# Kernel tuning notes

Hardware: AMD Instinct MI355X
Metric: run time of the kernel (lower is better)

Reference implementation:

```python
import jax, jax.numpy as jnp
import numpy as np
import math

IN_FEATURES = 3072
PADDED = 4096  # next power of two
ACT_BITS = 8
LN_EPS = 1e-6


def hadamard_transform(x):
    """Normalized fast Walsh-Hadamard transform along last dim (power of 2)."""
    n = x.shape[-1]
    m = n.bit_length() - 1  # log2(n)
    shape = x.shape
    y = x.reshape(shape[:-1] + (2,) * m)
    for ax in range(len(shape) - 1, len(shape) - 1 + m):
        a = jnp.take(y, 0, axis=ax)
        b = jnp.take(y, 1, axis=ax)
        y = jnp.stack([a + b, a - b], axis=ax)
    return y.reshape(shape) / jnp.sqrt(jnp.asarray(n, x.dtype))


def activation_quant(x, bits=ACT_BITS):
    """Per-token absmax int-b quant with STE (BitNet style)."""
    qb = 2 ** (bits - 1) - 1  # 127
    scale = qb / jnp.clip(jnp.max(jnp.abs(x), axis=-1, keepdims=True), 1e-5)
    q = jnp.clip(jnp.round(x * scale), -qb - 1, qb) / scale
    return x + jax.lax.stop_gradient(q - x)


def weight_quant(w):
    """Ternary absmean weight quant with STE (as in training path)."""
    scale = jnp.clip(jnp.mean(jnp.abs(w)), 1e-5)
    q = jnp.clip(jnp.round(w / scale), -1.0, 1.0) * scale
    return w + jax.lax.stop_gradient(q - w)


def layer_norm(x, gamma, beta, eps=LN_EPS):
    mu = jnp.mean(x, axis=-1, keepdims=True)
    var = jnp.mean(jnp.square(x - mu), axis=-1, keepdims=True)
    return (x - mu) * jax.lax.rsqrt(var + eps) * gamma + beta


def setup_inputs() -> dict:
    key = jax.random.key(0)
    k1, k2 = jax.random.split(key)
    x = jax.random.normal(k1, (4, 2048, IN_FEATURES), dtype=jnp.float32)
    ln_gamma = jnp.ones((IN_FEATURES,), dtype=jnp.float32)
    ln_beta = jnp.zeros((IN_FEATURES,), dtype=jnp.float32)
    weight = jax.random.normal(k2, (4096, PADDED), dtype=jnp.float32) * 0.02
    return {"x": x, "ln_gamma": ln_gamma, "ln_beta": ln_beta, "weight": weight}


def reference(x, ln_gamma, ln_beta, weight):
    x_norm = layer_norm(x, ln_gamma, ln_beta)
    pad = PADDED - IN_FEATURES
    x_pad = jnp.pad(x_norm, ((0, 0), (0, 0), (0, pad)))
    x_had = hadamard_transform(x_pad)
    x_q = activation_quant(x_had)
    w_q = weight_quant(weight)
    # F.linear: x @ W^T
    out = jnp.einsum('bsd,od->bso', x_q, w_q)
    return out
```

## Files before the change

### kernel.cpp

```cpp
#include <hip/hip_runtime.h>
#include <stdint.h>

#define TOKENS 8192
#define IN_F   3072
#define PAD_F  4096
#define N_OUT  4096
#define K_DIM  4096

using i32x4 = __attribute__((ext_vector_type(4))) int;

#define Q_OFF    0
#define WQ_OFF   33554432
#define AINV_OFF 50331648
#define PART_OFF 50364416
#define WSC_OFF  50380800

__device__ __forceinline__ void gload_lds16(const void* g, void* l) {
    __builtin_amdgcn_global_load_lds(
        (__attribute__((address_space(1))) void*)(void*)g,
        (__attribute__((address_space(3))) void*)l,
        16, 0, 0);
}

__global__ __launch_bounds__(256) void k_wabs(const float* __restrict__ w,
                                              float* __restrict__ partial) {
    int tid = threadIdx.x;
    const float4* w4 = (const float4*)(w + (size_t)blockIdx.x * 4096);
    float s = 0.f;
#pragma unroll
    for (int i = 0; i < 4; ++i) {
        float4 v = w4[tid + i * 256];
        s += fabsf(v.x) + fabsf(v.y) + fabsf(v.z) + fabsf(v.w);
    }
#pragma unroll
    for (int o = 32; o > 0; o >>= 1) s += __shfl_xor(s, o);
    __shared__ float rb[4];
    if ((tid & 63) == 0) rb[tid >> 6] = s;
    __syncthreads();
    if (tid == 0) partial[blockIdx.x] = rb[0] + rb[1] + rb[2] + rb[3];
}

__global__ __launch_bounds__(256) void k_wscale(const float* __restrict__ partial,
                                                float* __restrict__ wsp) {
    int tid = threadIdx.x;
    float s = 0.f;
#pragma unroll
    for (int i = 0; i < 16; ++i) s += partial[tid + i * 256];
#pragma unroll
    for (int o = 32; o > 0; o >>= 1) s += __shfl_xor(s, o);
    __shared__ float rb[4];
    if ((tid & 63) == 0) rb[tid >> 6] = s;
    __syncthreads();
    if (tid == 0)
        wsp[0] = fmaxf((rb[0] + rb[1] + rb[2] + rb[3]) * (1.0f / 16777216.0f), 1e-5f);
}

__global__ __launch_bounds__(256) void k_wquant(const float* __restrict__ w,
                                                const float* __restrict__ wsp,
                                                unsigned int* __restrict__ wq) {
    int idx = blockIdx.x * 256 + threadIdx.x;
    float ws = wsp[0];
    float4 v = ((const float4*)w)[idx];
    int a = (int)rintf(v.x / ws); a = max(-1, min(1, a));
    int b = (int)rintf(v.y / ws); b = max(-1, min(1, b));
    int c = (int)rintf(v.z / ws); c = max(-1, min(1, c));
    int d = (int)rintf(v.w / ws); d = max(-1, min(1, d));
    unsigned int p = (unsigned)(a & 255) | ((unsigned)(b & 255) << 8) |
                     ((unsigned)(c & 255) << 16) | ((unsigned)(d & 255) << 24);
    wq[idx] = p;
}

__global__ __launch_bounds__(256) void k_lnfwht(const float* __restrict__ x,
                                                const float* __restrict__ gamma,
                                                const float* __restrict__ beta,
                                                signed char* __restrict__ q,
                                                float* __restrict__ ainv) {
    __shared__ float s[PAD_F];
    __shared__ float rb[8];
    int tid = threadIdx.x;
    int lane = tid & 63;
    int t = blockIdx.x;
    const float4* xr4 = (const float4*)(x + (size_t)t * IN_F);
    const float4* g4  = (const float4*)gamma;
    const float4* b4  = (const float4*)beta;

    float v[16];
    float sum = 0.f;
#pragma unroll
    for (int i = 0; i < 3; ++i) {
        float4 xv = xr4[tid + i * 256];
        v[4 * i + 0] = xv.x; v[4 * i + 1] = xv.y;
        v[4 * i + 2] = xv.z; v[4 * i + 3] = xv.w;
        sum += xv.x + xv.y + xv.z + xv.w;
    }
    v[12] = v[13] = v[14] = v[15] = 0.f;
#pragma unroll
    for (int o = 32; o > 0; o >>= 1) sum += __shfl_xor(sum, o);
    if (lane == 0) rb[tid >> 6] = sum;
    __syncthreads();
    float mu = (rb[0] + rb[1] + rb[2] + rb[3]) * (1.0f / 3072.0f);

    float s2 = 0.f;
#pragma unroll
    for (int i = 0; i < 12; ++i) { float d = v[i] - mu; s2 += d * d; }
#pragma unroll
    for (int o = 32; o > 0; o >>= 1) s2 += __shfl_xor(s2, o);
    if (lane == 0) rb[4 + (tid >> 6)] = s2;
    __syncthreads();
    float var = (rb[4] + rb[5] + rb[6] + rb[7]) * (1.0f / 3072.0f);
    float rstd = 1.0f / sqrtf(var + 1e-6f);

#pragma unroll
    for (int i = 0; i < 3; ++i) {
        float4 gv = g4[tid + i * 256];
        float4 bv = b4[tid + i * 256];
        v[4 * i + 0] = (v[4 * i + 0] - mu) * rstd * gv.x + bv.x;
        v[4 * i + 1] = (v[4 * i + 1] - mu) * rstd * gv.y + bv.y;
        v[4 * i + 2] = (v[4 * i + 2] - mu) * rstd * gv.z + bv.z;
        v[4 * i + 3] = (v[4 * i + 3] - mu) * rstd * gv.w + bv.w;
    }

#pragma unroll
    for (int i = 0; i < 4; ++i) {
        float a0 = v[4 * i], a1 = v[4 * i + 1], a2 = v[4 * i + 2], a3 = v[4 * i + 3];
        float t0 = a0 + a1, t1 = a0 - a1, t2 = a2 + a3, t3 = a2 - a3;
        v[4 * i] = t0 + t2; v[4 * i + 1] = t1 + t3;
        v[4 * i + 2] = t0 - t2; v[4 * i + 3] = t1 - t3;
    }
#pragma unroll
    for (int c = 0; c < 4; ++c) {
        float a0 = v[c], a1 = v[4 + c], a2 = v[8 + c], a3 = v[12 + c];
        float t0 = a0 + a1, t1 = a0 - a1, t2 = a2 + a3, t3 = a2 - a3;
        v[c] = t0 + t2; v[4 + c] = t1 + t3;
        v[8 + c] = t0 - t2; v[12 + c] = t1 - t3;
    }
#pragma unroll
    for (int m = 1; m <= 32; m <<= 1) {
#pragma unroll
        for (int r = 0; r < 16; ++r) {
            float p = __shfl_xor(v[r], m);
            v[r] = (lane & m) ? (p - v[r]) : (v[r] + p);
        }
    }
#pragma unroll
    for (int m = 64; m <= 128; m <<= 1) {
        __syncthreads();
#pragma unroll
        for (int r = 0; r < 16; ++r) s[r * 256 + tid] = v[r];
        __syncthreads();
#pragma unroll
        for (int r = 0; r < 16; ++r) {
            float p = s[r * 256 + (tid ^ m)];
            v[r] = (tid & m) ? (p - v[r]) : (v[r] + p);
        }
    }

    float mx = 0.f;
#pragma unroll
    for (int r = 0; r < 16; ++r) mx = fmaxf(mx, fabsf(v[r]));
#pragma unroll
    for (int o = 32; o > 0; o >>= 1) mx = fmaxf(mx, __shfl_xor(mx, o));
    __syncthreads();
    if (lane == 0) rb[tid >> 6] = mx;
    __syncthreads();
    float amraw = fmaxf(fmaxf(rb[0], rb[1]), fmaxf(rb[2], rb[3]));
    float amax = fmaxf(amraw * (1.0f / 64.0f), 1e-5f);
    float scale = 127.0f / amax;
    if (tid == 0) ainv[t] = amax * (1.0f / 127.0f);

    unsigned int* qr = (unsigned int*)(q + (size_t)t * PAD_F);
#pragma unroll
    for (int i = 0; i < 4; ++i) {
        unsigned int pk = 0;
#pragma unroll
        for (int c = 0; c < 4; ++c) {
            int qi = (int)rintf(v[4 * i + c] * (1.0f / 64.0f) * scale);
            qi = max(-128, min(127, qi));
            pk |= (unsigned)(qi & 255) << (8 * c);
        }
        qr[tid + i * 256] = pk;
    }
}

#define BK 64
#define NT (K_DIM / BK)

#define VMW(n) asm volatile("s_waitcnt vmcnt(" #n ")" ::: "memory")

__global__ __launch_bounds__(512, 2) void k_gemm(const signed char* __restrict__ Aq,
                                                 const signed char* __restrict__ Wq,
                                                 const float* __restrict__ ainv,
                                                 const float* __restrict__ wsp,
                                                 float* __restrict__ out) {
    __shared__ signed char sA[4][128 * 128];
    __shared__ signed char sB[4][128 * 128];

    int tid = threadIdx.x;
    int lane = tid & 63, wid = tid >> 6;

    int bid = blockIdx.x;
    int xcd = bid & 7, li = bid >> 3;
    int bmb = xcd * 4 + (li & 3);
    int bnb = li >> 2;
    size_t bm0 = (size_t)bmb * 256, bn0 = (size_t)bnb * 256;

    int wm = wid >> 2, wn = wid & 3;

    int rr = lane >> 3, pp = lane & 7;
    int Lg = pp ^ rr;
    int spar = Lg >> 2, sh = Lg & 3;
    const signed char* gA = Aq + (bm0 + (size_t)(wid * 32 + 2 * rr + spar)) * K_DIM + sh * 16;
    const signed char* gB = Wq + (bn0 + (size_t)(wid * 32 + 2 * rr + spar)) * K_DIM + sh * 16;

    int fr = lane & 15, hh = lane >> 4;
    int pos = (((fr & 1) << 2) | hh) ^ (fr >> 1);
    int abase = (wm * 64 + (fr >> 1)) * 8 + pos;
    int bbase = (wn * 32 + (fr >> 1)) * 8 + pos;

    i32x4 acc[8][4];
#pragma unroll
    for (int m = 0; m < 8; ++m)
#pragma unroll
        for (int n = 0; n < 4; ++n) acc[m][n] = (i32x4){0, 0, 0, 0};

    i32x4 afA[8], bfA[4], afB[8], bfB[4];

    auto STAGE = [&](int b, int t) {
        size_t k0 = (size_t)t * BK;
        gload_lds16(gA + k0, &sA[b][(wid * 16) * 128]);
        gload_lds16(gA + k0 + (size_t)16 * K_DIM, &sA[b][(wid * 16 + 8) * 128]);
        gload_lds16(gB + k0, &sB[b][(wid * 16) * 128]);
        gload_lds16(gB + k0 + (size_t)16 * K_DIM, &sB[b][(wid * 16 + 8) * 128]);
    };

#define LOADF(B, AF, BF) do {                                           \
    const i32x4* va = (const i32x4*)&sA[B][0];                          \
    const i32x4* vb = (const i32x4*)&sB[B][0];                          \
    _Pragma("unroll")                                                   \
    for (int mf = 0; mf < 8; ++mf) AF[mf] = va[abase + mf * 64];        \
    _Pragma("unroll")                                                   \
    for (int nf = 0; nf < 4; ++nf) BF[nf] = vb[bbase + nf * 64];        \
} while (0)

#define COMPUTE(AF, BF) do {                                            \
    __builtin_amdgcn_s_setprio(1);                                      \
    _Pragma("unroll")                                                   \
    for (int mf = 0; mf < 8; ++mf)                                      \
        _Pragma("unroll")                                               \
        for (int nf = 0; nf < 4; ++nf)                                  \
            acc[mf][nf] = __builtin_amdgcn_mfma_i32_16x16x64_i8(        \
                AF[mf], BF[nf], acc[mf][nf], 0, 0, 0);                  \
    __builtin_amdgcn_s_setprio(0);                                      \
} while (0)

#define BODY(T, AFC, BFC, AFN, BFN) do {                                \
    STAGE((T + 3) & 3, T + 3);                                          \
    VMW(8);                                                             \
    __builtin_amdgcn_sched_barrier(0);                                  \
    __builtin_amdgcn_s_barrier();                                       \
    __builtin_amdgcn_sched_barrier(0);                                  \
    LOADF((T + 1) & 3, AFN, BFN);                                       \
    COMPUTE(AFC, BFC);                                                  \
    asm volatile("s_waitcnt lgkmcnt(0)" ::: "memory");                  \
    __builtin_amdgcn_sched_barrier(0);                                  \
} while (0)

    STAGE(0, 0);
    STAGE(1, 1);
    STAGE(2, 2);
    VMW(8);
    __builtin_amdgcn_sched_barrier(0);
    __builtin_amdgcn_s_barrier();
    __builtin_amdgcn_sched_barrier(0);
    LOADF(0, afA, bfA);
    asm volatile("s_waitcnt lgkmcnt(0)" ::: "memory");
    __builtin_amdgcn_sched_barrier(0);

#pragma unroll 1
    for (int t = 0; t < NT - 4; t += 2) {
        BODY(t, afA, bfA, afB, bfB);
        BODY(t + 1, afB, bfB, afA, bfA);
    }
    BODY(NT - 4, afA, bfA, afB, bfB);
    VMW(4);
    __builtin_amdgcn_sched_barrier(0);
    __builtin_amdgcn_s_barrier();
    __builtin_amdgcn_sched_barrier(0);
    LOADF(2, afA, bfA);
    COMPUTE(afB, bfB);
    asm volatile("s_waitcnt lgkmcnt(0)" ::: "memory");
    __builtin_amdgcn_sched_barrier(0);
    VMW(0);
    __builtin_amdgcn_sched_barrier(0);
    __builtin_amdgcn_s_barrier();
    __builtin_amdgcn_sched_barrier(0);
    LOADF(3, afB, bfB);
    COMPUTE(afA, bfA);
    asm volatile("s_waitcnt lgkmcnt(0)" ::: "memory");
    __builtin_amdgcn_sched_barrier(0);
    COMPUTE(afB, bfB);

    float wsc = wsp[0];
#pragma unroll
    for (int mf = 0; mf < 8; ++mf) {
        size_t row0 = bm0 + wm * 128 + mf * 16 + hh * 4;
#pragma unroll
        for (int r = 0; r < 4; ++r) {
            size_t row = row0 + r;
            float sa = wsc * ainv[row];
#pragma unroll
            for (int nf = 0; nf < 4; ++nf) {
                size_t col = bn0 + wn * 64 + nf * 16 + fr;
                out[row * N_OUT + col] = (float)acc[mf][nf][r] * sa;
            }
        }
    }
#undef LOADF
#undef COMPUTE
#undef BODY
}

extern "C" void kernel_launch(void* const* d_in, const int* in_sizes, int n_in,
                              void* d_out, int out_size, void* d_ws, size_t ws_size,
                              hipStream_t stream) {
    const float* x     = (const float*)d_in[0];
    const float* gamma = (const float*)d_in[1];
    const float* beta  = (const float*)d_in[2];
    const float* w     = (const float*)d_in[3];
    float* out = (float*)d_out;
    char* ws = (char*)d_ws;

    signed char* q   = (signed char*)(ws + Q_OFF);
    signed char* wq  = (signed char*)(ws + WQ_OFF);
    float* ainv      = (float*)(ws + AINV_OFF);
    float* partial   = (float*)(ws + PART_OFF);
    float* wsp       = (float*)(ws + WSC_OFF);

    k_wabs<<<dim3(4096), dim3(256), 0, stream>>>(w, partial);
    k_wscale<<<dim3(1), dim3(256), 0, stream>>>(partial, wsp);
    k_wquant<<<dim3(16384), dim3(256), 0, stream>>>(w, wsp, (unsigned int*)wq);
    k_lnfwht<<<dim3(TOKENS), dim3(256), 0, stream>>>(x, gamma, beta, q, ainv);
    k_gemm<<<dim3(512), dim3(512), 0, stream>>>(q, wq, ainv, wsp, out);
}
```

Baseline: 212.6 us.

## Restructure int8 GEMM main loop into two half-phases with single fragment set

Replaces the double-buffered register-fragment pipeline (prefetching the next tile's LDS fragments during compute) with a per-tile schedule split into two phases. Each phase loads part of the B fragments and issues half of the global-to-LDS stage, then runs half of the MFMAs, with extra workgroup barriers in between. This halves fragment register usage, which may ease register pressure, and interleaves memory issue with compute at a finer grain. The cost is that LDS reads are no longer overlapped with the previous tile's MFMAs, and there are more barriers per iteration.

```diff
diff --git a/kernel.cpp b/kernel.cpp
--- a/kernel.cpp
+++ b/kernel.cpp
@@ -186,6 +186,7 @@
 #define NT (K_DIM / BK)
 
 #define VMW(n) asm volatile("s_waitcnt vmcnt(" #n ")" ::: "memory")
+#define SB0()  __builtin_amdgcn_sched_barrier(0)
 
 __global__ __launch_bounds__(512, 2) void k_gemm(const signed char* __restrict__ Aq,
                                                  const signed char* __restrict__ Wq,
@@ -223,7 +224,7 @@
 #pragma unroll
         for (int n = 0; n < 4; ++n) acc[m][n] = (i32x4){0, 0, 0, 0};
 
-    i32x4 afA[8], bfA[4], afB[8], bfB[4];
+    i32x4 af[8], bf[4];
 
     auto STAGE = [&](int b, int t) {
         size_t k0 = (size_t)t * BK;
@@ -233,72 +234,72 @@
         gload_lds16(gB + k0 + (size_t)16 * K_DIM, &sB[b][(wid * 16 + 8) * 128]);
     };
 
-#define LOADF(B, AF, BF) do {                                           \
-    const i32x4* va = (const i32x4*)&sA[B][0];                          \
-    const i32x4* vb = (const i32x4*)&sB[B][0];                          \
+#define BODY(T, N, DS) do {                                             \
+    const i32x4* va = (const i32x4*)&sA[(T) & 3][0];                    \
+    const i32x4* vb = (const i32x4*)&sB[(T) & 3][0];                    \
+                     \
     _Pragma("unroll")                                                   \
-    for (int mf = 0; mf < 8; ++mf) AF[mf] = va[abase + mf * 64];        \
-    _Pragma("unroll")                                                   \
-    for (int nf = 0; nf < 4; ++nf) BF[nf] = vb[bbase + nf * 64];        \
-} while (0)
-
-#define COMPUTE(AF, BF) do {                                            \
+    for (int mf = 0; mf < 8; ++mf) af[mf] = va[abase + mf * 64];        \
+    bf[0] = vb[bbase];                                                  \
+    bf[1] = vb[bbase + 64];                                             \
+    if (DS) {                                                           \
+        size_t k0 = (size_t)((T) + 3) * BK;                             \
+        gload_lds16(gA + k0, &sA[((T) + 3) & 3][(wid * 16) * 128]);     \
+        gload_lds16(gA + k0 + (size_t)16 * K_DIM,                       \
+                    &sA[((T) + 3) & 3][(wid * 16 + 8) * 128]);          \
+    }                                                                   \
+    SB0();                                                              \
+    __builtin_amdgcn_s_barrier();                                       \
+    asm volatile("s_waitcnt lgkmcnt(0)" ::: "memory");                  \
+    SB0();                                                              \
     __builtin_amdgcn_s_setprio(1);                                      \
     _Pragma("unroll")                                                   \
-    for (int mf = 0; mf < 8; ++mf)                                      \
-        _Pragma("unroll")                                               \
-        for (int nf = 0; nf < 4; ++nf)                                  \
-            acc[mf][nf] = __builtin_amdgcn_mfma_i32_16x16x64_i8(        \
-                AF[mf], BF[nf], acc[mf][nf], 0, 0, 0);                  \
+    for (int mf = 0; mf < 8; ++mf) {                                    \
+        acc[mf][0] = __builtin_amdgcn_mfma_i32_16x16x64_i8(af[mf], bf[0], acc[mf][0], 0, 0, 0); \
+        acc[mf][1] = __builtin_amdgcn_mfma_i32_16x16x64_i8(af[mf], bf[1], acc[mf][1], 0, 0, 0); \
+    }                                                                   \
     __builtin_amdgcn_s_setprio(0);                                      \
-} while (0)
-
-#define BODY(T, AFC, BFC, AFN, BFN) do {                                \
-    STAGE((T + 3) & 3, T + 3);                                          \
-    VMW(8);                                                             \
-    __builtin_amdgcn_sched_barrier(0);                                  \
+    SB0();                                                              \
     __builtin_amdgcn_s_barrier();                                       \
-    __builtin_amdgcn_sched_barrier(0);                                  \
-    LOADF((T + 1) & 3, AFN, BFN);                                       \
-    COMPUTE(AFC, BFC);                                                  \
+               \
+    bf[2] = vb[bbase + 128];                                            \
+    bf[3] = vb[bbase + 192];                                            \
+    if (DS) {                                                           \
+        size_t k0 = (size_t)((T) + 3) * BK;                             \
+        gload_lds16(gB + k0, &sB[((T) + 3) & 3][(wid * 16) * 128]);     \
+        gload_lds16(gB + k0 + (size_t)16 * K_DIM,                       \
+                    &sB[((T) + 3) & 3][(wid * 16 + 8) * 128]);          \
+    }                                                                   \
+    VMW(N);                                                             \
+    SB0();                                                              \
+    __builtin_amdgcn_s_barrier();                                       \
     asm volatile("s_waitcnt lgkmcnt(0)" ::: "memory");                  \
-    __builtin_amdgcn_sched_barrier(0);                                  \
+    SB0();                                                              \
+    __builtin_amdgcn_s_setprio(1);                                      \
+    _Pragma("unroll")                                                   \
+    for (int mf = 0; mf < 8; ++mf) {                                    \
+        acc[mf][2] = __builtin_amdgcn_mfma_i32_16x16x64_i8(af[mf], bf[2], acc[mf][2], 0, 0, 0); \
+        acc[mf][3] = __builtin_amdgcn_mfma_i32_16x16x64_i8(af[mf], bf[3], acc[mf][3], 0, 0, 0); \
+    }                                                                   \
+    __builtin_amdgcn_s_setprio(0);                                      \
+    SB0();                                                              \
+    __builtin_amdgcn_s_barrier();                                       \
+    SB0();                                                              \
 } while (0)
 
     STAGE(0, 0);
     STAGE(1, 1);
     STAGE(2, 2);
     VMW(8);
-    __builtin_amdgcn_sched_barrier(0);
+    SB0();
     __builtin_amdgcn_s_barrier();
-    __builtin_amdgcn_sched_barrier(0);
-    LOADF(0, afA, bfA);
-    asm volatile("s_waitcnt lgkmcnt(0)" ::: "memory");
-    __builtin_amdgcn_sched_barrier(0);
+    SB0();
 
 #pragma unroll 1
-    for (int t = 0; t < NT - 4; t += 2) {
-        BODY(t, afA, bfA, afB, bfB);
-        BODY(t + 1, afB, bfB, afA, bfA);
-    }
-    BODY(NT - 4, afA, bfA, afB, bfB);
-    VMW(4);
-    __builtin_amdgcn_sched_barrier(0);
-    __builtin_amdgcn_s_barrier();
-    __builtin_amdgcn_sched_barrier(0);
-    LOADF(2, afA, bfA);
-    COMPUTE(afB, bfB);
-    asm volatile("s_waitcnt lgkmcnt(0)" ::: "memory");
-    __builtin_amdgcn_sched_barrier(0);
-    VMW(0);
-    __builtin_amdgcn_sched_barrier(0);
-    __builtin_amdgcn_s_barrier();
-    __builtin_amdgcn_sched_barrier(0);
-    LOADF(3, afB, bfB);
-    COMPUTE(afA, bfA);
-    asm volatile("s_waitcnt lgkmcnt(0)" ::: "memory");
-    __builtin_amdgcn_sched_barrier(0);
-    COMPUTE(afB, bfB);
+    for (int t = 0; t < NT - 3; ++t) BODY(t, 8, true);
+    BODY(NT - 3, 4, false);
+    BODY(NT - 2, 0, false);
+    BODY(NT - 1, 0, false);
 
     float wsc = wsp[0];
 #pragma unroll
@@ -315,8 +316,6 @@
             }
         }
     }
-#undef LOADF
-#undef COMPUTE
 #undef BODY
 }
 
```

Result: no change. 213.8 us (+0.6%).
